# Performance work log

Measured on AMD Instinct MI355X. Metric: run time of the kernel, lower is better.

The kernel has to match this reference:

```python
import jax, jax.numpy as jnp
import numpy as np

B, T, J, K = 4, 16, 20, 300
N_CROP, N_FULL = 2048, 16384
D_TRAJ, D_OBJ, D_EMB, D_JF = 9, 256, 64, 64
RADIUS = 0.025


def _skew(v):
    x, y, z = v[..., 0], v[..., 1], v[..., 2]
    o = jnp.zeros_like(x)
    return jnp.stack([jnp.stack([o, -z, y], -1),
                      jnp.stack([z, o, -x], -1),
                      jnp.stack([-y, x, o], -1)], -2)


def _rot_align(a, b, eps=1e-8):
    # rotation matrices aligning direction a -> b (Rodrigues), shapes [...,3]
    a = a / (jnp.linalg.norm(a, axis=-1, keepdims=True) + eps)
    b = b / (jnp.linalg.norm(b, axis=-1, keepdims=True) + eps)
    v = jnp.cross(a, b)
    c = jnp.sum(a * b, -1)
    s2 = jnp.sum(v * v, -1)
    vx = _skew(v)
    I = jnp.eye(3, dtype=a.dtype)
    R = I + vx + jnp.matmul(vx, vx) * ((1.0 - c) / (s2 + eps))[..., None, None]
    return jnp.where((s2 < eps)[..., None, None], I, R)


def _ik_solver_mano(joints, template):
    # joints, template: [N,21,3] -> (joints, per-joint SE(3) [N,21,4,4])
    R = _rot_align(template - template[:, :1], joints - joints[:, :1])
    R = R.at[:, 0].set(jnp.eye(3, dtype=joints.dtype))
    t = joints - jnp.einsum('njxy,njy->njx', R, template)
    G = jnp.zeros(joints.shape[:2] + (4, 4), joints.dtype)
    G = G.at[..., :3, :3].set(R).at[..., :3, 3].set(t).at[..., 3, 3].set(1.0)
    return joints, G


def _ball_query(q, pts, k, radius):
    # q [N,J,3], pts [N,P,3] -> (ind [N,J,k] padded with -1, mask [N,J,k])
    # first-k-in-original-order points within radius, like pytorch3d.ball_query
    P = pts.shape[1]
    d2 = jnp.sum((q[:, :, None] - pts[:, None]) ** 2, -1)  # [N,J,P]
    within = d2 < radius * radius
    ar = jnp.arange(P, dtype=jnp.int32)
    key = jnp.where(within, ar, ar + P)  # unique keys -> stable ordering
    idx = jnp.argsort(key, axis=-1)[..., :k].astype(jnp.int32)
    ok = jnp.take_along_axis(within, idx, axis=-1)
    return jnp.where(ok, idx, -1), ok


def _forward(rhand_traj, obj_crop, obj_full, template_joints,
             W_obj, b_obj, W_init, b_init, W_emb, b_emb, W_jf, b_jf, W_st):
    BT = B * T
    # obj_encoder stand-in: shared linear + relu + max-pool over points
    oc = obj_crop.reshape(BT, -1, 6)
    obj_feat = jnp.max(jax.nn.relu(oc @ W_obj + b_obj), axis=1)  # [BT,D_OBJ]
    feat = jnp.concatenate([rhand_traj.reshape(BT, -1), obj_feat], -1)
    joints = (feat @ W_init + b_init).reshape(BT, J, 3)
    joints_init_out = joints.reshape(B, T, J, 3)
    joints21 = jnp.concatenate([jnp.zeros((BT, 1, 3), joints.dtype), joints], 1)
    joints21, G = _ik_solver_mano(joints21, jnp.broadcast_to(template_joints, (BT, 21, 3)))
    jcano = joints21[:, 1:]           # [BT,J,3]
    G = G[:, 1:]                      # [BT,J,4,4]
    joint_embed = (jcano @ W_emb + b_emb).transpose(0, 2, 1)  # [BT,D_EMB,J]
    of = obj_full.reshape(BT, -1, 6)
    ind, mask = _ball_query(jcano, of[..., :3], K, RADIUS)    # [BT,J,K]
    gidx = jnp.where(ind < 0, of.shape[1] - 1, ind)           # torch -1 indexing == last
    samp = of[jnp.arange(BT)[:, None, None], gidx]            # [BT,J,K,6] gather
    Ginv = jnp.linalg.inv(G)
    homo = jnp.concatenate([samp[..., :3], jnp.ones(samp.shape[:-1] + (1,), samp.dtype)], -1)
    p = jnp.einsum('bjxy,bjky->bjkx', Ginv, homo)
    cano_p = p[..., :3] / p[..., 3:4]
    cano_n = jnp.einsum('bjxy,bjky->bjkx', Ginv[..., :3, :3], samp[..., 3:6])
    sp = jnp.concatenate([cano_p, cano_n], -1)                # [BT,J,K,6]
    # joint_feat_extractor stand-in: per-joint masked pointnet
    f = jax.nn.relu(sp @ W_jf + b_jf)                         # [BT,J,K,D_JF]
    f = jnp.max(jnp.where(mask[..., None], f, -jnp.inf), axis=2)
    f = jnp.where(jnp.isfinite(f), f, 0.0)                    # [BT,J,D_JF]
    joint_feat = jnp.concatenate([joint_embed, f.transpose(0, 2, 1)], 1)  # [BT,D,J]
    jf = joint_feat.reshape(B, T, -1, J).transpose(1, 2, 0, 3)            # [T,D,B,J]
    disp_cano = jnp.einsum('tdbj,dk->btjk', jf, W_st)                     # [B,T,J,3]
    disp = jnp.einsum('bjxy,bjy->bjx', G[..., :3, :3],
                      disp_cano.reshape(BT, J, 3)).reshape(B, T, J, 3)
    disp = disp - jax.lax.stop_gradient(joints_init_out) \
                + jax.lax.stop_gradient(jcano.reshape(B, T, J, 3))
    return joints_init_out, disp


def setup_inputs() -> dict:
    key = jax.random.key(0)
    ks = jax.random.split(key, 9)
    rhand_traj = jax.random.normal(ks[0], (B, T, D_TRAJ), jnp.float32)

    def pts(k, n):
        xyz = jax.random.normal(k, (B, T, n, 3), jnp.float32) * 0.1
        nrm = jax.random.normal(jax.random.fold_in(k, 1), (B, T, n, 3), jnp.float32)
        nrm = nrm / (jnp.linalg.norm(nrm, axis=-1, keepdims=True) + 1e-8)
        return jnp.concatenate([xyz, nrm], -1)

    obj_crop = pts(ks[1], N_CROP)
    obj_full = pts(ks[2], N_FULL)
    template = jax.random.normal(ks[3], (1, 21, 3), jnp.float32) * 0.05
    template = template - template[:, :1]  # center_idx=0 (wrist at origin)
    W_obj = jax.random.normal(ks[4], (6, D_OBJ), jnp.float32) * 0.1
    b_obj = jnp.zeros((D_OBJ,), jnp.float32)
    W_init = jax.random.normal(ks[5], (D_TRAJ + D_OBJ, J * 3), jnp.float32) * 0.002
    b_init = jnp.zeros((J * 3,), jnp.float32)
    W_emb = jax.random.normal(ks[6], (3, D_EMB), jnp.float32) * 0.1
    b_emb = jnp.zeros((D_EMB,), jnp.float32)
    W_jf = jax.random.normal(ks[7], (6, D_JF), jnp.float32) * 0.1
    b_jf = jnp.zeros((D_JF,), jnp.float32)
    W_st = jax.random.normal(ks[8], (D_EMB + D_JF, 3), jnp.float32) * 0.05
    return dict(rhand_traj=rhand_traj, obj_crop=obj_crop, obj_full=obj_full,
                template_joints=template, W_obj=W_obj, b_obj=b_obj,
                W_init=W_init, b_init=b_init, W_emb=W_emb, b_emb=b_emb,
                W_jf=W_jf, b_jf=b_jf, W_st=W_st)


def reference(rhand_traj, obj_crop, obj_full, template_joints,
              W_obj, b_obj, W_init, b_init, W_emb, b_emb, W_jf, b_jf, W_st):
    return _forward(rhand_traj, obj_crop, obj_full, template_joints,
                    W_obj, b_obj, W_init, b_init, W_emb, b_emb, W_jf, b_jf, W_st)
```

## Files before the change

kernel.cpp:

```cpp
#include <hip/hip_runtime.h>
#include <math.h>

#define BTC   64
#define NJ    20
#define KSEL  300
#define NCROP 2048
#define NFULL 16384
#define DOBJ  256
#define DEMB  64
#define DJF   64
#define RAD2  (0.025f*0.025f)

__global__ __launch_bounds__(256) void k_objfeat_part(
    const float* __restrict__ obj_crop,
    const float* __restrict__ W_obj,
    const float* __restrict__ b_obj,
    float* __restrict__ ws_partial)
{
    const int bt = blockIdx.x >> 4;
    const int ch = blockIdx.x & 15;
    const int t  = threadIdx.x;
    __shared__ float lds_pts[128 * 8];

    float wo[6];
#pragma unroll
    for (int i = 0; i < 6; ++i) wo[i] = W_obj[i * DOBJ + t];
    const float bo = b_obj[t];

    const float* base = obj_crop + (size_t)bt * NCROP * 6 + ch * 768;
#pragma unroll
    for (int i = 0; i < 3; ++i) {
        const int idx = i * 256 + t;
        lds_pts[(idx / 6) * 8 + (idx % 6)] = base[idx];
    }
    __syncthreads();

    float mx = 0.0f;
#pragma unroll 8
    for (int p = 0; p < 128; ++p) {
        const float4 lo = *(const float4*)(lds_pts + p * 8);
        const float2 hi = *(const float2*)(lds_pts + p * 8 + 4);
        float acc = bo;
        acc += lo.x * wo[0]; acc += lo.y * wo[1]; acc += lo.z * wo[2];
        acc += lo.w * wo[3]; acc += hi.x * wo[4]; acc += hi.y * wo[5];
        mx = fmaxf(mx, fmaxf(acc, 0.0f));
    }
    ws_partial[(bt * 16 + ch) * 256 + t] = mx;
}

__global__ __launch_bounds__(256) void k_joints_ik(
    const float* __restrict__ ws_partial,
    const float* __restrict__ traj,
    const float* __restrict__ W_init,
    const float* __restrict__ b_init,
    const float* __restrict__ tmpl,
    float* __restrict__ out_joints,
    float* __restrict__ ws_joints,
    float* __restrict__ ws_R,
    float* __restrict__ ws_Rinv,
    float* __restrict__ ws_tinv)
{
    const int bt = blockIdx.x;
    const int t  = threadIdx.x;
    __shared__ float feat[272];
    __shared__ float jarr[60];

    const float* pp = ws_partial + bt * 16 * 256 + t;
    float mx = pp[0];
#pragma unroll
    for (int c = 1; c < 16; ++c) mx = fmaxf(mx, pp[c * 256]);
    feat[9 + t] = mx;
    if (t < 9) feat[t] = traj[bt * 9 + t];
    __syncthreads();

    if (t < 240) {
        const int o = t >> 2, r = t & 3;
        float acc = 0.0f;
#pragma unroll
        for (int m = 0; m < 66; ++m) {
            const int i = r + 4 * m;
            acc += feat[i] * W_init[i * 60 + o];
        }
        if (r == 0) acc += feat[264] * W_init[264 * 60 + o];
        acc += __shfl_xor(acc, 1);
        acc += __shfl_xor(acc, 2);
        if (r == 0) jarr[o] = acc + b_init[o];
    }
    __syncthreads();

    if (t < 60) {
        out_joints[bt * 60 + t] = jarr[t];
        ws_joints[bt * 60 + t]  = jarr[t];
    }

    if (t < NJ) {
        const int j   = t;
        const int gid = bt * NJ + j;
        const float eps = 1e-8f;
        float bx0 = jarr[j * 3 + 0];
        float by0 = jarr[j * 3 + 1];
        float bz0 = jarr[j * 3 + 2];
        float ax0 = tmpl[(j + 1) * 3 + 0] - tmpl[0];
        float ay0 = tmpl[(j + 1) * 3 + 1] - tmpl[1];
        float az0 = tmpl[(j + 1) * 3 + 2] - tmpl[2];

        float ia = 1.0f / (sqrtf(ax0 * ax0 + ay0 * ay0 + az0 * az0) + eps);
        float ax = ax0 * ia, ay = ay0 * ia, az = az0 * ia;
        float ib = 1.0f / (sqrtf(bx0 * bx0 + by0 * by0 + bz0 * bz0) + eps);
        float bx = bx0 * ib, by = by0 * ib, bz = bz0 * ib;

        float vx = ay * bz - az * by;
        float vy = az * bx - ax * bz;
        float vz = ax * by - ay * bx;
        float cc = ax * bx + ay * by + az * bz;
        float s2 = vx * vx + vy * vy + vz * vz;

        float R[9];
        if (s2 < eps) {
            R[0]=1; R[1]=0; R[2]=0; R[3]=0; R[4]=1; R[5]=0; R[6]=0; R[7]=0; R[8]=1;
        } else {
            float coef = (1.0f - cc) / (s2 + eps);
            R[0] = 1.0f + coef * (-(vy * vy + vz * vz));
            R[1] = -vz  + coef * (vx * vy);
            R[2] =  vy  + coef * (vx * vz);
            R[3] =  vz  + coef * (vx * vy);
            R[4] = 1.0f + coef * (-(vx * vx + vz * vz));
            R[5] = -vx  + coef * (vy * vz);
            R[6] = -vy  + coef * (vx * vz);
            R[7] =  vx  + coef * (vy * vz);
            R[8] = 1.0f + coef * (-(vx * vx + vy * vy));
        }
        float tx = bx0 - (R[0] * ax0 + R[1] * ay0 + R[2] * az0);
        float ty = by0 - (R[3] * ax0 + R[4] * ay0 + R[5] * az0);
        float tz = bz0 - (R[6] * ax0 + R[7] * ay0 + R[8] * az0);

        float det = R[0] * (R[4] * R[8] - R[5] * R[7])
                  - R[1] * (R[3] * R[8] - R[5] * R[6])
                  + R[2] * (R[3] * R[7] - R[4] * R[6]);
        float id = 1.0f / det;
        float Ri[9];
        Ri[0] = (R[4] * R[8] - R[5] * R[7]) * id;
        Ri[1] = (R[2] * R[7] - R[1] * R[8]) * id;
        Ri[2] = (R[1] * R[5] - R[2] * R[4]) * id;
        Ri[3] = (R[5] * R[6] - R[3] * R[8]) * id;
        Ri[4] = (R[0] * R[8] - R[2] * R[6]) * id;
        Ri[5] = (R[2] * R[3] - R[0] * R[5]) * id;
        Ri[6] = (R[3] * R[7] - R[4] * R[6]) * id;
        Ri[7] = (R[1] * R[6] - R[0] * R[7]) * id;
        Ri[8] = (R[0] * R[4] - R[1] * R[3]) * id;

        float tix = -(Ri[0] * tx + Ri[1] * ty + Ri[2] * tz);
        float tiy = -(Ri[3] * tx + Ri[4] * ty + Ri[5] * tz);
        float tiz = -(Ri[6] * tx + Ri[7] * ty + Ri[8] * tz);

#pragma unroll
        for (int i = 0; i < 9; ++i) ws_R[gid * 9 + i] = R[i];
#pragma unroll
        for (int i = 0; i < 9; ++i) ws_Rinv[gid * 9 + i] = Ri[i];
        ws_tinv[gid * 3 + 0] = tix;
        ws_tinv[gid * 3 + 1] = tiy;
        ws_tinv[gid * 3 + 2] = tiz;
    }
}

__global__ __launch_bounds__(256) void k_ballmask(
    const float* __restrict__ obj_full,
    const float* __restrict__ ws_joints,
    unsigned long long* __restrict__ ws_mask)
{
    const int bt   = blockIdx.x >> 5;
    const int blkc = blockIdx.x & 31;
    const int t    = threadIdx.x;
    const int lane = t & 63;
    const int wv   = t >> 6;

    __shared__ unsigned long long lmask[NJ][8];

    float jx[NJ], jy[NJ], jz[NJ];
    const float* jp = ws_joints + bt * NJ * 3;
#pragma unroll
    for (int j = 0; j < NJ; ++j) {
        jx[j] = jp[j * 3 + 0];
        jy[j] = jp[j * 3 + 1];
        jz[j] = jp[j * 3 + 2];
    }

    const float* blk = obj_full + ((size_t)bt * NFULL + blkc * 512) * 6;
#pragma unroll
    for (int it = 0; it < 2; ++it) {
        const float* p = blk + (size_t)(it * 256 + t) * 6;
        const float2 xy = *(const float2*)p;
        const float  pz = p[2];
        const float px = xy.x, py = xy.y;
        const int word = it * 4 + wv;
#pragma unroll
        for (int j = 0; j < NJ; ++j) {
            float dx = px - jx[j], dy = py - jy[j], dz = pz - jz[j];
            bool within = (dx * dx + dy * dy + dz * dz) < RAD2;
            unsigned long long m = __ballot(within);
            if (lane == 0) lmask[j][word] = m;
        }
    }
    __syncthreads();

    if (t < NJ * 8) {
        const int j = t >> 3, w = t & 7;
        ws_mask[(size_t)(bt * NJ + j) * 256 + blkc * 8 + w] = lmask[j][w];
    }
}

__global__ __launch_bounds__(256) void k_ballq_disp(
    const float* __restrict__ obj_full,
    const unsigned long long* __restrict__ ws_mask,
    const float* __restrict__ ws_joints,
    const float* __restrict__ ws_R,
    const float* __restrict__ ws_Rinv,
    const float* __restrict__ ws_tinv,
    const float* __restrict__ W_jf,
    const float* __restrict__ b_jf,
    const float* __restrict__ W_emb,
    const float* __restrict__ b_emb,
    const float* __restrict__ W_st,
    float* __restrict__ out)
{
    const int pair = blockIdx.x;
    const int bt   = pair / NJ;
    const int t    = threadIdx.x;
    const int lane = t & 63;
    const int wv   = t >> 6;

    __shared__ float sel[KSEL * 6];
    __shared__ int   wsum[4];
    __shared__ float red[256];

    const float qx = ws_joints[pair * 3 + 0];
    const float qy = ws_joints[pair * 3 + 1];
    const float qz = ws_joints[pair * 3 + 2];
    float Ri[9];
#pragma unroll
    for (int i = 0; i < 9; ++i) Ri[i] = ws_Rinv[pair * 9 + i];
    const float tix = ws_tinv[pair * 3 + 0];
    const float tiy = ws_tinv[pair * 3 + 1];
    const float tiz = ws_tinv[pair * 3 + 2];

    const float* pts = obj_full + (size_t)bt * NFULL * 6;

    unsigned long long myw = ws_mask[(size_t)pair * 256 + t];

    int cnt = __popcll(myw);
    int incl = cnt;
#pragma unroll
    for (int o = 1; o < 64; o <<= 1) {
        int v = __shfl_up(incl, o);
        if (lane >= o) incl += v;
    }
    if (lane == 63) wsum[wv] = incl;
    __syncthreads();
    int wbase = 0;
    for (int w = 0; w < wv; ++w) wbase += wsum[w];
    const int excl = wbase + incl - cnt;
    const int total = wsum[0] + wsum[1] + wsum[2] + wsum[3];

    if (excl < KSEL && cnt > 0) {
        unsigned long long m = myw;
        int r = excl;
        while (m && r < KSEL) {
            int b = __ffsll((long long)m) - 1;
            m &= m - 1;
            const float* p = pts + (size_t)(t * 64 + b) * 6;
            float px = p[0], py = p[1], pz = p[2];
            float nx = p[3], ny = p[4], nz = p[5];
            sel[r * 6 + 0] = Ri[0] * px + Ri[1] * py + Ri[2] * pz + tix;
            sel[r * 6 + 1] = Ri[3] * px + Ri[4] * py + Ri[5] * pz + tiy;
            sel[r * 6 + 2] = Ri[6] * px + Ri[7] * py + Ri[8] * pz + tiz;
            sel[r * 6 + 3] = Ri[0] * nx + Ri[1] * ny + Ri[2] * nz;
            sel[r * 6 + 4] = Ri[3] * nx + Ri[4] * ny + Ri[5] * nz;
            sel[r * 6 + 5] = Ri[6] * nx + Ri[7] * ny + Ri[8] * nz;
            ++r;
        }
    }
    __syncthreads();

    const int n   = total < KSEL ? total : KSEL;
    const int chn = t & 63;
    const int sl  = t >> 6;
    float wj[6];
#pragma unroll
    for (int i = 0; i < 6; ++i) wj[i] = W_jf[i * DJF + chn];
    const float bj = b_jf[chn];

    float acc = 0.0f;
    for (int p = sl; p < n; p += 4) {
        float v = bj;
#pragma unroll
        for (int i = 0; i < 6; ++i) v += sel[p * 6 + i] * wj[i];
        acc = fmaxf(acc, fmaxf(v, 0.0f));
    }
    red[t] = acc;
    __syncthreads();

    if (t < 64) {
        float mm = fmaxf(fmaxf(red[t], red[t + 64]),
                         fmaxf(red[t + 128], red[t + 192]));
        float e = b_emb[t] + qx * W_emb[t] + qy * W_emb[64 + t] + qz * W_emb[128 + t];
        float g0 = e * W_st[t * 3 + 0] + mm * W_st[(64 + t) * 3 + 0];
        float g1 = e * W_st[t * 3 + 1] + mm * W_st[(64 + t) * 3 + 1];
        float g2 = e * W_st[t * 3 + 2] + mm * W_st[(64 + t) * 3 + 2];
#pragma unroll
        for (int o = 32; o > 0; o >>= 1) {
            g0 += __shfl_xor(g0, o);
            g1 += __shfl_xor(g1, o);
            g2 += __shfl_xor(g2, o);
        }
        if (t == 0) {
            const float* R = ws_R + pair * 9;
            out[3840 + pair * 3 + 0] = R[0] * g0 + R[1] * g1 + R[2] * g2;
            out[3840 + pair * 3 + 1] = R[3] * g0 + R[4] * g1 + R[5] * g2;
            out[3840 + pair * 3 + 2] = R[6] * g0 + R[7] * g1 + R[8] * g2;
        }
    }
}

extern "C" void kernel_launch(void* const* d_in, const int* in_sizes, int n_in,
                              void* d_out, int out_size, void* d_ws, size_t ws_size,
                              hipStream_t stream) {
    const float* rhand_traj = (const float*)d_in[0];
    const float* obj_crop   = (const float*)d_in[1];
    const float* obj_full   = (const float*)d_in[2];
    const float* tmpl       = (const float*)d_in[3];
    const float* W_obj      = (const float*)d_in[4];
    const float* b_obj      = (const float*)d_in[5];
    const float* W_init     = (const float*)d_in[6];
    const float* b_init     = (const float*)d_in[7];
    const float* W_emb      = (const float*)d_in[8];
    const float* b_emb      = (const float*)d_in[9];
    const float* W_jf       = (const float*)d_in[10];
    const float* b_jf       = (const float*)d_in[11];
    const float* W_st       = (const float*)d_in[12];
    float* out = (float*)d_out;

    float* ws = (float*)d_ws;
    float* ws_partial = ws;
    float* ws_joints  = ws + 262144;
    float* ws_R       = ws + 265984;
    float* ws_Rinv    = ws + 277504;
    float* ws_tinv    = ws + 289024;
    unsigned long long* ws_mask =
        (unsigned long long*)(ws + 292864);

    k_objfeat_part<<<BTC * 16, 256, 0, stream>>>(obj_crop, W_obj, b_obj, ws_partial);
    k_joints_ik<<<BTC, 256, 0, stream>>>(ws_partial, rhand_traj, W_init, b_init,
                                         tmpl, out, ws_joints,
                                         ws_R, ws_Rinv, ws_tinv);
    k_ballmask<<<BTC * 32, 256, 0, stream>>>(obj_full, ws_joints, ws_mask);
    k_ballq_disp<<<BTC * NJ, 256, 0, stream>>>(obj_full, ws_mask, ws_joints,
                                               ws_R, ws_Rinv, ws_tinv,
                                               W_jf, b_jf, W_emb, b_emb, W_st, out);
}
```

Baseline: 37.85 us.

## Restructure object feature kernel to 64-thread blocks computing four channels each

```diff
diff --git a/kernel.cpp b/kernel.cpp
--- a/kernel.cpp
+++ b/kernel.cpp
@@ -11,41 +11,56 @@
 #define DJF   64
 #define RAD2  (0.025f*0.025f)
 
-__global__ __launch_bounds__(256) void k_objfeat_part(
+__global__ __launch_bounds__(64) void k_objfeat_part(
     const float* __restrict__ obj_crop,
     const float* __restrict__ W_obj,
     const float* __restrict__ b_obj,
     float* __restrict__ ws_partial)
 {
-    const int bt = blockIdx.x >> 4;
-    const int ch = blockIdx.x & 15;
-    const int t  = threadIdx.x;
-    __shared__ float lds_pts[128 * 8];
-
-    float wo[6];
-#pragma unroll
-    for (int i = 0; i < 6; ++i) wo[i] = W_obj[i * DOBJ + t];
-    const float bo = b_obj[t];
-
-    const float* base = obj_crop + (size_t)bt * NCROP * 6 + ch * 768;
-#pragma unroll
-    for (int i = 0; i < 3; ++i) {
-        const int idx = i * 256 + t;
-        lds_pts[(idx / 6) * 8 + (idx % 6)] = base[idx];
-    }
-    __syncthreads();
-
-    float mx = 0.0f;
+    const int bt  = blockIdx.x >> 5;
+    const int blk = blockIdx.x & 31;
+    const int t   = threadIdx.x;
+    __shared__ float lds_pts[64 * 8];
+
+    float wo[4][6], bo[4];
+#pragma unroll
+    for (int k = 0; k < 4; ++k) {
+        const int ch = k * 64 + t;
+#pragma unroll
+        for (int i = 0; i < 6; ++i) wo[k][i] = W_obj[i * DOBJ + ch];
+        bo[k] = b_obj[ch];
+    }
+
+    const float* src = obj_crop + (size_t)bt * NCROP * 6 + blk * 384;
+#pragma unroll
+    for (int i = 0; i < 6; ++i) {
+        const int idx = i * 64 + t;
+        lds_pts[(idx / 6) * 8 + (idx % 6)] = src[idx];
+    }
+    __syncthreads();
+
+    float mx0 = 0.0f, mx1 = 0.0f, mx2 = 0.0f, mx3 = 0.0f;
 #pragma unroll 8
-    for (int p = 0; p < 128; ++p) {
+    for (int p = 0; p < 64; ++p) {
         const float4 lo = *(const float4*)(lds_pts + p * 8);
         const float2 hi = *(const float2*)(lds_pts + p * 8 + 4);
-        float acc = bo;
-        acc += lo.x * wo[0]; acc += lo.y * wo[1]; acc += lo.z * wo[2];
-        acc += lo.w * wo[3]; acc += hi.x * wo[4]; acc += hi.y * wo[5];
-        mx = fmaxf(mx, fmaxf(acc, 0.0f));
-    }
-    ws_partial[(bt * 16 + ch) * 256 + t] = mx;
+        float a0 = bo[0], a1 = bo[1], a2 = bo[2], a3 = bo[3];
+        a0 += lo.x * wo[0][0]; a1 += lo.x * wo[1][0]; a2 += lo.x * wo[2][0]; a3 += lo.x * wo[3][0];
+        a0 += lo.y * wo[0][1]; a1 += lo.y * wo[1][1]; a2 += lo.y * wo[2][1]; a3 += lo.y * wo[3][1];
+        a0 += lo.z * wo[0][2]; a1 += lo.z * wo[1][2]; a2 += lo.z * wo[2][2]; a3 += lo.z * wo[3][2];
+        a0 += lo.w * wo[0][3]; a1 += lo.w * wo[1][3]; a2 += lo.w * wo[2][3]; a3 += lo.w * wo[3][3];
+        a0 += hi.x * wo[0][4]; a1 += hi.x * wo[1][4]; a2 += hi.x * wo[2][4]; a3 += hi.x * wo[3][4];
+        a0 += hi.y * wo[0][5]; a1 += hi.y * wo[1][5]; a2 += hi.y * wo[2][5]; a3 += hi.y * wo[3][5];
+        mx0 = fmaxf(mx0, fmaxf(a0, 0.0f));
+        mx1 = fmaxf(mx1, fmaxf(a1, 0.0f));
+        mx2 = fmaxf(mx2, fmaxf(a2, 0.0f));
+        mx3 = fmaxf(mx3, fmaxf(a3, 0.0f));
+    }
+    float* dst = ws_partial + (size_t)(bt * 32 + blk) * 256;
+    dst[t]       = mx0;
+    dst[64 + t]  = mx1;
+    dst[128 + t] = mx2;
+    dst[192 + t] = mx3;
 }
 
 __global__ __launch_bounds__(256) void k_joints_ik(
@@ -65,10 +80,10 @@
     __shared__ float feat[272];
     __shared__ float jarr[60];
 
-    const float* pp = ws_partial + bt * 16 * 256 + t;
+    const float* pp = ws_partial + (size_t)bt * 32 * 256 + t;
     float mx = pp[0];
 #pragma unroll
-    for (int c = 1; c < 16; ++c) mx = fmaxf(mx, pp[c * 256]);
+    for (int c = 1; c < 32; ++c) mx = fmaxf(mx, pp[c * 256]);
     feat[9 + t] = mx;
     if (t < 9) feat[t] = traj[bt * 9 + t];
     __syncthreads();
@@ -341,14 +356,14 @@
 
     float* ws = (float*)d_ws;
     float* ws_partial = ws;
-    float* ws_joints  = ws + 262144;
-    float* ws_R       = ws + 265984;
-    float* ws_Rinv    = ws + 277504;
-    float* ws_tinv    = ws + 289024;
+    float* ws_joints  = ws + 524288;
+    float* ws_R       = ws + 528128;
+    float* ws_Rinv    = ws + 539648;
+    float* ws_tinv    = ws + 551168;
     unsigned long long* ws_mask =
-        (unsigned long long*)(ws + 292864);
-
-    k_objfeat_part<<<BTC * 16, 256, 0, stream>>>(obj_crop, W_obj, b_obj, ws_partial);
+        (unsigned long long*)(ws + 555008);
+
+    k_objfeat_part<<<BTC * 32, 64, 0, stream>>>(obj_crop, W_obj, b_obj, ws_partial);
     k_joints_ik<<<BTC, 256, 0, stream>>>(ws_partial, rhand_traj, W_init, b_init,
                                          tmpl, out, ws_joints,
                                          ws_R, ws_Rinv, ws_tinv);
```

Result: slower. 43.39 us (+14.6%).
